# Optimization experiments

Hardware: AMD Instinct MI355X
Metric: run time of the kernel (lower is better)

Reference implementation:

```python
import jax, jax.numpy as jnp
import numpy as np

C = 66  # channels (joints)
NB_CLASSES = 14
T = 96


def conv1d(x, w, b, pad, groups=1):
    # x: (N, Cin, L), w: (Cout, Cin//groups, K)
    y = jax.lax.conv_general_dilated(
        x, w, window_strides=(1,), padding=[(pad, pad)],
        feature_group_count=groups, dimension_numbers=('NCH', 'OIH', 'NCH'))
    return y + b[None, :, None]


def pool2(x):
    # AvgPool1d(kernel_size=2) along last axis
    return x.reshape(*x.shape[:-1], x.shape[-1] // 2, 2).mean(-1)


def setup_inputs() -> dict:
    key = jax.random.key(0)
    ks = jax.random.split(key, 16)

    def xavier(k, shape, fan_in, fan_out, gain=jnp.sqrt(2.0)):
        bound = gain * jnp.sqrt(6.0 / (fan_in + fan_out))
        return jax.random.uniform(k, shape, jnp.float32, -bound, bound)

    B = 2048
    x = jax.random.normal(ks[0], (B, T, C), jnp.float32)
    # shared convs (same weights for every channel)
    w_hs = xavier(ks[1], (8, 1, 7), 1 * 7, 8 * 7)
    b_hs = jnp.full((8,), 0.1, jnp.float32)
    w_ls = xavier(ks[2], (8, 1, 3), 1 * 3, 8 * 3)
    b_ls = jnp.full((8,), 0.1, jnp.float32)
    # per-channel individual convs, packed for grouped conv (groups=C)
    w_hi1 = xavier(ks[3], (C * 4, 8, 7), 8 * 7, 4 * 7)
    b_hi1 = jnp.full((C * 4,), 0.1, jnp.float32)
    w_hi2 = xavier(ks[4], (C * 4, 4, 7), 4 * 7, 4 * 7)
    b_hi2 = jnp.full((C * 4,), 0.1, jnp.float32)
    w_li1 = xavier(ks[5], (C * 4, 8, 3), 8 * 3, 4 * 3)
    b_li1 = jnp.full((C * 4,), 0.1, jnp.float32)
    w_li2 = xavier(ks[6], (C * 4, 4, 3), 4 * 3, 4 * 3)
    b_li2 = jnp.full((C * 4,), 0.1, jnp.float32)
    # MLP
    F_IN = 9 * C * 12
    w_fc1 = xavier(ks[7], (1936, F_IN), F_IN, 1936)
    b_fc1 = jnp.full((1936,), 0.1, jnp.float32)
    w_fc2 = xavier(ks[8], (NB_CLASSES, 1936), 1936, NB_CLASSES)
    b_fc2 = jnp.full((NB_CLASSES,), 0.1, jnp.float32)
    return dict(x=x, w_hs=w_hs, b_hs=b_hs, w_ls=w_ls, b_ls=b_ls,
                w_hi1=w_hi1, b_hi1=b_hi1, w_hi2=w_hi2, b_hi2=b_hi2,
                w_li1=w_li1, b_li1=b_li1, w_li2=w_li2, b_li2=b_li2,
                w_fc1=w_fc1, b_fc1=b_fc1, w_fc2=w_fc2, b_fc2=b_fc2)


def _branch(xc_flat, B, w_s, b_s, w_i1, b_i1, w_i2, b_i2, pad):
    # xc_flat: (B*C, 1, T). Shared conv applied per channel, then grouped
    # (per-channel) convs with groups=C.
    h = pool2(jax.nn.relu(conv1d(xc_flat, w_s, b_s, pad)))       # (B*C, 8, 48)
    h = h.reshape(B, C * 8, T // 2)
    h = pool2(jax.nn.relu(conv1d(h, w_i1, b_i1, pad, groups=C)))  # (B, C*4, 24)
    h = pool2(jax.nn.relu(conv1d(h, w_i2, b_i2, pad, groups=C)))  # (B, C*4, 12)
    return h.reshape(B, C, 4, T // 8)


def reference(x, w_hs, b_hs, w_ls, b_ls, w_hi1, b_hi1, w_hi2, b_hi2,
              w_li1, b_li1, w_li2, b_li2, w_fc1, b_fc1, w_fc2, b_fc2):
    B = x.shape[0]
    xc = jnp.transpose(x, (0, 2, 1))            # (B, C, T)
    xc_flat = xc.reshape(B * C, 1, T)
    high = _branch(xc_flat, B, w_hs, b_hs, w_hi1, b_hi1, w_hi2, b_hi2, pad=3)
    low = _branch(xc_flat, B, w_ls, b_ls, w_li1, b_li1, w_li2, b_li2, pad=1)
    orig = pool2(pool2(pool2(xc)))[:, :, None, :]  # (B, C, 1, 12)
    # per-channel concat order: [original, low, high] -> (B, C, 9, 12)
    feat = jnp.concatenate([orig, low, high], axis=2).reshape(B, 9 * C * 12)
    h = jax.nn.relu(feat @ w_fc1.T + b_fc1)
    return h @ w_fc2.T + b_fc2
```

## Files before the change

kernel.cpp:

```cpp
#include <hip/hip_runtime.h>
#include <hip/hip_bf16.h>

#define T_LEN 96
#define C_CH  66
#define FIN   7128
#define KPAD  7168
#define NFC1  1936
#define NPAD  2048
#define NCLS  14

typedef __bf16 bf16x8 __attribute__((ext_vector_type(8)));
typedef float  f32x4  __attribute__((ext_vector_type(4)));

#define GLD_LDS(gp, lp) __builtin_amdgcn_global_load_lds(                     \
    (__attribute__((address_space(1))) void*)(gp),                            \
    (__attribute__((address_space(3))) void*)(lp), 16, 0, 0)

__global__ __launch_bounds__(256) void transpose_kernel(
    const float* __restrict__ x, float* __restrict__ xT, int B)
{
    __shared__ float tile[64][65];
    const int t = threadIdx.x & 63;
    const int w = threadIdx.x >> 6;
    const int tc0 = blockIdx.x * 64;
    const int b0  = blockIdx.y * 64;
    #pragma unroll
    for (int j = 0; j < 16; j++) {
        const int r = w * 16 + j;
        tile[r][t] = x[(size_t)(b0 + r) * (T_LEN * C_CH) + tc0 + t];
    }
    __syncthreads();
    #pragma unroll
    for (int j = 0; j < 16; j++) {
        const int r = w * 16 + j;
        xT[(size_t)(tc0 + r) * B + b0 + t] = tile[t][r];
    }
}

__global__ __launch_bounds__(256) void pad_w_kernel(
    const float* __restrict__ w, __hip_bfloat16* __restrict__ wb)
{
    int idx = blockIdx.x * 256 + threadIdx.x;
    int row = idx / 896;
    int cc  = idx - row * 896;
    float4 a = {0.f, 0.f, 0.f, 0.f}, b = {0.f, 0.f, 0.f, 0.f};
    if (row < NFC1 && cc < 891) {
        const float4* src = (const float4*)(w + (size_t)row * FIN + cc * 8);
        a = src[0];
        b = src[1];
    }
    __align__(16) __hip_bfloat16 v[8];
    v[0] = __float2bfloat16(a.x); v[1] = __float2bfloat16(a.y);
    v[2] = __float2bfloat16(a.z); v[3] = __float2bfloat16(a.w);
    v[4] = __float2bfloat16(b.x); v[5] = __float2bfloat16(b.y);
    v[6] = __float2bfloat16(b.z); v[7] = __float2bfloat16(b.w);
    *(int4*)(wb + (size_t)row * KPAD + cc * 8) = *(const int4*)v;
}

template <int K, bool DO_EXTRA>
__device__ __forceinline__ void conv_branch(
    const float* __restrict__ xb, int ts,
    const float* __restrict__ wS, const float* __restrict__ bS,
    const float* __restrict__ wi1, const float* __restrict__ bi1,
    const float* __restrict__ wi2, const float* __restrict__ bi2,
    __hip_bfloat16* __restrict__ frow, int out_off)
{
    constexpr int PAD = K / 2;
    constexpr int XW  = 24 + 6 * PAD;
    constexpr int THW = 12 + 2 * PAD;

    float s2phR[4][24];

    #pragma unroll
    for (int tt = 0; tt < 4; tt++) {
        float xw[XW];
        #pragma unroll
        for (int i = 0; i < XW; i++) {
            const int t = 24 * tt - 3 * PAD + i;
            xw[i] = (t >= 0 && t < T_LEN) ? xb[(size_t)t * ts] : 0.f;
        }

        if (DO_EXTRA) {
            #pragma unroll
            for (int r = 0; r < 3; r++) {
                float s = 0.f;
                #pragma unroll
                for (int k = 0; k < 8; k++) s += xw[3 * PAD + 8 * r + k];
                frow[3 * tt + r] = __float2bfloat16(s * 0.125f);
            }
        }

        float s2a[4][12];
        #pragma unroll
        for (int oc = 0; oc < 4; oc++) {
            const float bv = bi1[oc];
            #pragma unroll
            for (int q = 0; q < 12; q++) s2a[oc][q] = bv;
        }

        #pragma unroll 1
        for (int ic = 0; ic < 8; ic++) {
            const float bs1 = bS[ic];
            float thw[THW];
            #pragma unroll
            for (int j = 0; j < THW; j++) {
                const int jg = 12 * tt - PAD + j;
                if (jg < 0 || jg >= 48) { thw[j] = 0.f; continue; }
                float y0 = bs1, y1 = bs1;
                #pragma unroll
                for (int k = 0; k < K; k++) {
                    const float w = wS[ic * K + k];
                    y0 = fmaf(w, xw[2 * j + k], y0);
                    y1 = fmaf(w, xw[2 * j + 1 + k], y1);
                }
                thw[j] = 0.5f * (fmaxf(y0, 0.f) + fmaxf(y1, 0.f));
            }
            #pragma unroll
            for (int q = 0; q < 12; q++) {
                #pragma unroll
                for (int oc = 0; oc < 4; oc++) {
                    float a = s2a[oc][q];
                    #pragma unroll
                    for (int k = 0; k < K; k++)
                        a = fmaf(wi1[(oc * 8 + ic) * K + k], thw[q + k], a);
                    s2a[oc][q] = a;
                }
            }
        }

        #pragma unroll
        for (int oc = 0; oc < 4; oc++)
            #pragma unroll
            for (int r = 0; r < 6; r++)
                s2phR[oc][6 * tt + r] =
                    0.5f * (fmaxf(s2a[oc][2 * r], 0.f) +
                            fmaxf(s2a[oc][2 * r + 1], 0.f));
    }

    #pragma unroll 1
    for (int oc = 0; oc < 4; oc++) {
        const float bv = bi2[oc];
        #pragma unroll
        for (int q = 0; q < 12; q++) {
            float y0 = bv, y1 = bv;
            #pragma unroll
            for (int ic = 0; ic < 4; ic++) {
                #pragma unroll
                for (int k = 0; k < K; k++) {
                    const float w = wi2[(oc * 4 + ic) * K + k];
                    const int i0 = 2 * q + k - PAD;
                    const int i1 = 2 * q + 1 + k - PAD;
                    if (i0 >= 0 && i0 < 24) y0 = fmaf(w, s2phR[ic][i0], y0);
                    if (i1 >= 0 && i1 < 24) y1 = fmaf(w, s2phR[ic][i1], y1);
                }
            }
            frow[out_off + oc * 12 + q] =
                __float2bfloat16(0.5f * (fmaxf(y0, 0.f) + fmaxf(y1, 0.f)));
        }
    }
}

__global__ __launch_bounds__(64, 2) void conv_fused_kernel(
    const float* __restrict__ x, int ts, int bs, int cs,
    const float* __restrict__ w_hs, const float* __restrict__ b_hs,
    const float* __restrict__ w_ls, const float* __restrict__ b_ls,
    const float* __restrict__ w_hi1, const float* __restrict__ b_hi1,
    const float* __restrict__ w_hi2, const float* __restrict__ b_hi2,
    const float* __restrict__ w_li1, const float* __restrict__ b_li1,
    const float* __restrict__ w_li2, const float* __restrict__ b_li2,
    __hip_bfloat16* __restrict__ feat)
{
    const int lane = threadIdx.x;
    const int b = blockIdx.x * 64 + lane;
    const int c = blockIdx.y;
    const float* xb = x + (size_t)b * bs + (size_t)c * cs;
    __hip_bfloat16* frow = feat + (size_t)b * KPAD + c * 108;

    if (blockIdx.z == 0) {
        conv_branch<7, false>(xb, ts, w_hs, b_hs,
                              w_hi1 + c * 224, b_hi1 + c * 4,
                              w_hi2 + c * 112, b_hi2 + c * 4, frow, 60);
    } else {
        if (c == 0) {
            int4* tail = (int4*)(feat + (size_t)b * KPAD + FIN);
            const int4 z = {0, 0, 0, 0};
            #pragma unroll
            for (int i = 0; i < 5; i++) tail[i] = z;
        }
        conv_branch<3, true>(xb, ts, w_ls, b_ls,
                             w_li1 + c * 96, b_li1 + c * 4,
                             w_li2 + c * 48, b_li2 + c * 4, frow, 12);
    }
}

__global__ __launch_bounds__(512, 2) void gemm_kernel(
    const __hip_bfloat16* __restrict__ A,
    const __hip_bfloat16* __restrict__ Bw,
    float* __restrict__ Cm, int kchunk)
{
    __shared__ __align__(16) __hip_bfloat16 As[8192];
    __shared__ __align__(16) __hip_bfloat16 Bs[8192];

    const int tid  = threadIdx.x;
    const int lane = tid & 63;
    const int wid  = tid >> 6;
    const int m0 = blockIdx.y * 256;
    const int n0 = blockIdx.x * 256;
    const int wm = (wid >> 2) * 128;
    const int wn = (wid & 3) * 64;
    const int lr = lane & 15;
    const int quad = lane >> 4;

    const int r0 = tid >> 2, c0 = (tid & 3) * 8;
    const __hip_bfloat16* gA0 = A  + (size_t)(m0 + r0) * KPAD + c0;
    const __hip_bfloat16* gA1 = gA0 + (size_t)128 * KPAD;
    const __hip_bfloat16* gB0 = Bw + (size_t)(n0 + r0) * KPAD + c0;
    const __hip_bfloat16* gB1 = gB0 + (size_t)128 * KPAD;
    __hip_bfloat16* lA0 = As + wid * 512;
    __hip_bfloat16* lA1 = As + 4096 + wid * 512;
    __hip_bfloat16* lB0 = Bs + wid * 512;
    __hip_bfloat16* lB1 = Bs + 4096 + wid * 512;

    f32x4 acc[8][4] = {};

    const int kBeg = blockIdx.z * kchunk;
    const int kEnd = kBeg + kchunk;
    for (int k0 = kBeg; k0 < kEnd; k0 += 32) {
        __syncthreads();
        GLD_LDS(gA0 + k0, lA0);
        GLD_LDS(gA1 + k0, lA1);
        GLD_LDS(gB0 + k0, lB0);
        GLD_LDS(gB1 + k0, lB1);
        __syncthreads();
        bf16x8 af[8], bfr[4];
        #pragma unroll
        for (int mt = 0; mt < 8; mt++)
            af[mt] = *(const bf16x8*)(As + (wm + mt * 16 + lr) * 32 + quad * 8);
        #pragma unroll
        for (int nt = 0; nt < 4; nt++)
            bfr[nt] = *(const bf16x8*)(Bs + (wn + nt * 16 + lr) * 32 + quad * 8);
        #pragma unroll
        for (int mt = 0; mt < 8; mt++)
            #pragma unroll
            for (int nt = 0; nt < 4; nt++)
                acc[mt][nt] = __builtin_amdgcn_mfma_f32_16x16x32_bf16(
                    af[mt], bfr[nt], acc[mt][nt], 0, 0, 0);
    }

    float* Cs = Cm + (size_t)blockIdx.z * NPAD * NPAD;
    #pragma unroll
    for (int mt = 0; mt < 8; mt++) {
        #pragma unroll
        for (int nt = 0; nt < 4; nt++) {
            const int col = n0 + wn + nt * 16 + lr;
            const int rb  = m0 + wm + mt * 16 + quad * 4;
            #pragma unroll
            for (int r = 0; r < 4; r++)
                Cs[(size_t)(rb + r) * NPAD + col] = acc[mt][nt][r];
        }
    }
}

__global__ __launch_bounds__(256) void fc2_kernel(
    const float* __restrict__ h1, const float* __restrict__ b1,
    const float* __restrict__ w2, const float* __restrict__ b2,
    float* __restrict__ out, int nslab)
{
    const int b = blockIdx.x;
    const int tid = threadIdx.x;
    float acc[NCLS];
    #pragma unroll
    for (int o = 0; o < NCLS; o++) acc[o] = 0.f;
    for (int n = tid; n < NFC1; n += 256) {
        float hv = b1[n];
        for (int s = 0; s < nslab; s++)
            hv += h1[(size_t)s * NPAD * NPAD + (size_t)b * NPAD + n];
        float h = fmaxf(hv, 0.f);
        #pragma unroll
        for (int o = 0; o < NCLS; o++)
            acc[o] = fmaf(h, w2[o * NFC1 + n], acc[o]);
    }
    __shared__ float red[4][NCLS];
    #pragma unroll
    for (int o = 0; o < NCLS; o++) {
        float v = acc[o];
        #pragma unroll
        for (int s = 32; s > 0; s >>= 1) v += __shfl_down(v, s);
        if ((tid & 63) == 0) red[tid >> 6][o] = v;
    }
    __syncthreads();
    if (tid < NCLS)
        out[b * NCLS + tid] = red[0][tid] + red[1][tid] + red[2][tid] +
                              red[3][tid] + b2[tid];
}

extern "C" void kernel_launch(void* const* d_in, const int* in_sizes, int n_in,
                              void* d_out, int out_size, void* d_ws, size_t ws_size,
                              hipStream_t stream)
{
    (void)n_in; (void)out_size;
    const float* x     = (const float*)d_in[0];
    const float* w_hs  = (const float*)d_in[1];
    const float* b_hs  = (const float*)d_in[2];
    const float* w_ls  = (const float*)d_in[3];
    const float* b_ls  = (const float*)d_in[4];
    const float* w_hi1 = (const float*)d_in[5];
    const float* b_hi1 = (const float*)d_in[6];
    const float* w_hi2 = (const float*)d_in[7];
    const float* b_hi2 = (const float*)d_in[8];
    const float* w_li1 = (const float*)d_in[9];
    const float* b_li1 = (const float*)d_in[10];
    const float* w_li2 = (const float*)d_in[11];
    const float* b_li2 = (const float*)d_in[12];
    const float* w_fc1 = (const float*)d_in[13];
    const float* b_fc1 = (const float*)d_in[14];
    const float* w_fc2 = (const float*)d_in[15];
    const float* b_fc2 = (const float*)d_in[16];
    float* out = (float*)d_out;

    const int B = in_sizes[0] / (T_LEN * C_CH);

    char* ws = (char*)d_ws;
    const size_t featB = (size_t)B * KPAD * 2;
    const size_t wbB   = (size_t)NPAD * KPAD * 2;
    const size_t slabB = (size_t)NPAD * NPAD * 4;
    const size_t xtB   = (size_t)T_LEN * C_CH * B * 4;
    const size_t base2 = featB + wbB;

    __hip_bfloat16* feat = (__hip_bfloat16*)ws;
    __hip_bfloat16* wb   = (__hip_bfloat16*)(ws + featB);
    float* h1            = (float*)(ws + base2);

    const int sk = (ws_size >= base2 + 4 * slabB) ? 4 : 2;
    const bool use_xt = (ws_size >= base2 + sk * slabB + xtB);
    float* xT = (float*)(ws + base2 + sk * slabB);

    pad_w_kernel<<<dim3((NPAD * 896) / 256), 256, 0, stream>>>(w_fc1, wb);

    const float* cx = x;
    int ts = C_CH, bsi = T_LEN * C_CH, cs = 1;
    if (use_xt) {
        transpose_kernel<<<dim3(99, B / 64), 256, 0, stream>>>(x, xT, B);
        cx = xT; ts = C_CH * B; bsi = 1; cs = B;
    }
    conv_fused_kernel<<<dim3(B / 64, C_CH, 2), 64, 0, stream>>>(
        cx, ts, bsi, cs, w_hs, b_hs, w_ls, b_ls,
        w_hi1, b_hi1, w_hi2, b_hi2, w_li1, b_li1, w_li2, b_li2, feat);
    gemm_kernel<<<dim3(NPAD / 256, B / 256, sk), 512, 0, stream>>>(
        feat, wb, h1, KPAD / sk);
    fc2_kernel<<<dim3(B), 256, 0, stream>>>(h1, b_fc1, w_fc2, b_fc2, out, sk);
}
```

Baseline: 440.1 us.

## Double-buffer GEMM LDS tiles with K=64 prefetch of next tile

Restructures the fc1 bf16 MFMA GEMM main loop into a two-stage pipeline. The next 64-wide K slice of A and B is issued with global_load_lds into the alternate buffer while MFMAs run on the current one. This cuts the barriers per K step from two to one and doubles the K depth per iteration. LDS use grows to 128 KB per block, which likely prevents the two blocks per CU that the launch bounds target. The 128-byte row stride may also add LDS bank conflicts on fragment reads, and kchunk must now be a multiple of 64.

Measured after the change: 415.3 us. 1.06x faster.

```diff
diff --git a/kernel.cpp b/kernel.cpp
--- a/kernel.cpp
+++ b/kernel.cpp
@@ -198,8 +198,7 @@
     const __hip_bfloat16* __restrict__ Bw,
     float* __restrict__ Cm, int kchunk)
 {
-    __shared__ __align__(16) __hip_bfloat16 As[8192];
-    __shared__ __align__(16) __hip_bfloat16 Bs[8192];
+    __shared__ __align__(16) __hip_bfloat16 lds[2][2][256 * 64];
 
     const int tid  = threadIdx.x;
     const int lane = tid & 63;
@@ -211,52 +210,68 @@
     const int lr = lane & 15;
     const int quad = lane >> 4;
 
-    const int r0 = tid >> 2, c0 = (tid & 3) * 8;
-    const __hip_bfloat16* gA0 = A  + (size_t)(m0 + r0) * KPAD + c0;
-    const __hip_bfloat16* gA1 = gA0 + (size_t)128 * KPAD;
-    const __hip_bfloat16* gB0 = Bw + (size_t)(n0 + r0) * KPAD + c0;
-    const __hip_bfloat16* gB1 = gB0 + (size_t)128 * KPAD;
-    __hip_bfloat16* lA0 = As + wid * 512;
-    __hip_bfloat16* lA1 = As + 4096 + wid * 512;
-    __hip_bfloat16* lB0 = Bs + wid * 512;
-    __hip_bfloat16* lB1 = Bs + 4096 + wid * 512;
+    const int srow = tid >> 3, scol = (tid & 7) * 8;
+    const __hip_bfloat16* gA = A  + (size_t)(m0 + srow) * KPAD + scol;
+    const __hip_bfloat16* gB = Bw + (size_t)(n0 + srow) * KPAD + scol;
 
     f32x4 acc[8][4] = {};
 
     const int kBeg = blockIdx.z * kchunk;
-    const int kEnd = kBeg + kchunk;
-    for (int k0 = kBeg; k0 < kEnd; k0 += 32) {
+    const int numt = kchunk >> 6;
+
+    #pragma unroll
+    for (int r = 0; r < 4; r++) {
+        GLD_LDS(gA + (size_t)r * 64 * KPAD + kBeg,
+                &lds[0][0][r * 4096 + wid * 512]);
+        GLD_LDS(gB + (size_t)r * 64 * KPAD + kBeg,
+                &lds[0][1][r * 4096 + wid * 512]);
+    }
+    __syncthreads();
+
+    for (int t = 0; t < numt; ++t) {
+        const int cb = t & 1;
+        if (t + 1 < numt) {
+            const int k1 = kBeg + (t + 1) * 64;
+            #pragma unroll
+            for (int r = 0; r < 4; r++) {
+                GLD_LDS(gA + (size_t)r * 64 * KPAD + k1,
+                        &lds[cb ^ 1][0][r * 4096 + wid * 512]);
+                GLD_LDS(gB + (size_t)r * 64 * KPAD + k1,
+                        &lds[cb ^ 1][1][r * 4096 + wid * 512]);
+            }
+        }
+        const __hip_bfloat16* As_ = &lds[cb][0][0];
+        const __hip_bfloat16* Bs_ = &lds[cb][1][0];
+        #pragma unroll
+        for (int ks = 0; ks < 2; ks++) {
+            bf16x8 bfr[4];
+            #pragma unroll
+            for (int nn = 0; nn < 4; nn++)
+                bfr[nn] = *(const bf16x8*)(Bs_ + ((wn + nn * 16 + lr) << 6) +
+                                           ks * 32 + quad * 8);
+            #pragma unroll
+            for (int mt = 0; mt < 8; mt++) {
+                const bf16x8 af = *(const bf16x8*)(As_ +
+                        ((wm + mt * 16 + lr) << 6) + ks * 32 + quad * 8);
+                #pragma unroll
+                for (int nn = 0; nn < 4; nn++)
+                    acc[mt][nn] = __builtin_amdgcn_mfma_f32_16x16x32_bf16(
+                        af, bfr[nn], acc[mt][nn], 0, 0, 0);
+            }
+        }
         __syncthreads();
-        GLD_LDS(gA0 + k0, lA0);
-        GLD_LDS(gA1 + k0, lA1);
-        GLD_LDS(gB0 + k0, lB0);
-        GLD_LDS(gB1 + k0, lB1);
-        __syncthreads();
-        bf16x8 af[8], bfr[4];
-        #pragma unroll
-        for (int mt = 0; mt < 8; mt++)
-            af[mt] = *(const bf16x8*)(As + (wm + mt * 16 + lr) * 32 + quad * 8);
-        #pragma unroll
-        for (int nt = 0; nt < 4; nt++)
-            bfr[nt] = *(const bf16x8*)(Bs + (wn + nt * 16 + lr) * 32 + quad * 8);
-        #pragma unroll
-        for (int mt = 0; mt < 8; mt++)
-            #pragma unroll
-            for (int nt = 0; nt < 4; nt++)
-                acc[mt][nt] = __builtin_amdgcn_mfma_f32_16x16x32_bf16(
-                    af[mt], bfr[nt], acc[mt][nt], 0, 0, 0);
     }
 
     float* Cs = Cm + (size_t)blockIdx.z * NPAD * NPAD;
     #pragma unroll
     for (int mt = 0; mt < 8; mt++) {
         #pragma unroll
-        for (int nt = 0; nt < 4; nt++) {
-            const int col = n0 + wn + nt * 16 + lr;
+        for (int nn = 0; nn < 4; nn++) {
+            const int col = n0 + wn + nn * 16 + lr;
             const int rb  = m0 + wm + mt * 16 + quad * 4;
             #pragma unroll
             for (int r = 0; r < 4; r++)
-                Cs[(size_t)(rb + r) * NPAD + col] = acc[mt][nt][r];
+                Cs[(size_t)(rb + r) * NPAD + col] = acc[mt][nn][r];
         }
     }
 }
```
